# Optimization experiments

Hardware: AMD Instinct MI355X
Metric: run time of the kernel (lower is better)

## Reference

```python
import jax, jax.numpy as jnp
import numpy as np

B, N, V, F, H, O, NCONV = 4096, 64, 100, 128, 256, 1, 4
NEG_SLOPE = 0.01  # torch nn.LeakyReLU default


def leaky(x):
    return jnp.where(x >= 0, x, NEG_SLOPE * x)


def setup_inputs() -> dict:
    key = jax.random.key(0)
    ks = jax.random.split(key, 16)
    node_mat = jax.random.normal(ks[0], (B, N, V), dtype=jnp.float32)
    a = (jax.random.uniform(ks[1], (B, N, N)) < 0.15).astype(jnp.float32)
    adj_mat = jnp.maximum(a, jnp.swapaxes(a, 1, 2))
    s = 0.05
    params = dict(
        W_init=s * jax.random.normal(ks[2], (V, F), jnp.float32),
        b_init=jnp.zeros((F,), jnp.float32),
        W_conv=s * jax.random.normal(ks[3], (NCONV, F, F), jnp.float32),
        b_conv=jnp.zeros((NCONV, F), jnp.float32),
        W_fc0=s * jax.random.normal(ks[4], (F, H), jnp.float32),
        b_fc0=jnp.zeros((H,), jnp.float32),
        W_fc1=s * jax.random.normal(ks[5], (H, H), jnp.float32),
        b_fc1=jnp.zeros((H,), jnp.float32),
        W_out=s * jax.random.normal(ks[6], (H, O), jnp.float32),
        b_out=jnp.zeros((O,), jnp.float32),
    )
    return dict(node_mat=node_mat, adj_mat=adj_mat, **params)


def reference(node_mat, adj_mat, W_init, b_init, W_conv, b_conv,
              W_fc0, b_fc0, W_fc1, b_fc1, W_out, b_out):
    # init transform + LeakyReLU
    x = leaky(node_mat @ W_init + b_init)                      # [B, N, F]
    # degree-normalized adjacency: diag(1/deg) @ A == row-scale (exact same math
    # as the original eye-expand + double bmm, without the NxN diagonal matmul)
    deg = jnp.clip(adj_mat.sum(axis=-1, keepdims=True), 1.0, None)  # [B, N, 1]
    A_norm = adj_mat / deg                                     # [B, N, N]
    for i in range(W_conv.shape[0]):
        agg = jnp.einsum('bij,bjf->bif', A_norm, x)            # neighbor mean
        x = leaky(agg @ W_conv[i] + b_conv[i])
    # mean pooling over atoms
    g = x.mean(axis=1)                                         # [B, F]
    # fc head (dropout p=0 -> identity)
    h = leaky(g @ W_fc0 + b_fc0)
    h = leaky(h @ W_fc1 + b_fc1)
    return h @ W_out + b_out                                   # [B, O]
```

## Files before the change

kernel.cpp:

```cpp
#include <hip/hip_runtime.h>

#define NATOMS 64
#define VDIM 100
#define FDIM 128
#define HDIM 256
#define NCONV 4

typedef __bf16 bf16x8 __attribute__((ext_vector_type(8)));
typedef __bf16 bf16x4 __attribute__((ext_vector_type(4)));
typedef float f32x4 __attribute__((ext_vector_type(4)));

__device__ __forceinline__ float lrelu(float x) {
  return x >= 0.0f ? x : 0.01f * x;
}

__global__ void prep_weights(const float* __restrict__ Wi,
                             const float* __restrict__ Wc,
                             __bf16* __restrict__ WtI,
                             __bf16* __restrict__ WtC) {
  int idx = blockIdx.x * 256 + threadIdx.x;
  int e = idx & 7;
  int lane = (idx >> 3) & 63;
  int ks = (idx >> 9) & 3;
  int n16 = (idx >> 11) & 7;
  int l = idx >> 14;
  int n = n16 * 16 + (lane & 15);
  int k = ks * 32 + (lane >> 4) * 8 + e;
  if (l == 0) {
    WtI[idx] = (__bf16)(k < VDIM ? Wi[k * FDIM + n] : 0.0f);
  } else {
    WtC[(l - 1) * 16384 + (idx & 16383)] =
        (__bf16)Wc[(l - 1) * FDIM * FDIM + k * FDIM + n];
  }
}

template <bool PRODUCE_FRAG>
__device__ __forceinline__ void conv_step(
    const __bf16* __restrict__ Wt, const float* __restrict__ bias,
    const __bf16* __restrict__ sRow, bf16x8 xfrag[2][2], float psum[2],
    const int w, const int lane) {
  const int lr = lane & 15;
  const int g = lane >> 4;
  const int k0 = g * 8;
  f32x4 acc[2][4];
#pragma unroll
  for (int ni = 0; ni < 2; ++ni)
#pragma unroll
    for (int mi = 0; mi < 4; ++mi) acc[ni][mi] = {0.f, 0.f, 0.f, 0.f};
#pragma unroll
  for (int ks = 0; ks < 4; ++ks) {
    bf16x8 bfrag[2], afrag[4];
#pragma unroll
    for (int ni = 0; ni < 2; ++ni)
      bfrag[ni] = *(const bf16x8*)&Wt[(((2 * w + ni) * 4 + ks) * 64 + lane) * 8];
#pragma unroll
    for (int mi = 0; mi < 4; ++mi) {
      int m = mi * 16 + lr;
      afrag[mi] = *(const bf16x8*)&sRow[m * 128 + ((ks * 32 + k0) ^ ((m & 7) << 3))];
    }
#pragma unroll
    for (int ni = 0; ni < 2; ++ni)
#pragma unroll
      for (int mi = 0; mi < 4; ++mi)
        acc[ni][mi] = __builtin_amdgcn_mfma_f32_16x16x32_bf16(
            afrag[mi], bfrag[ni], acc[ni][mi], 0, 0, 0);
  }
#pragma unroll
  for (int ni = 0; ni < 2; ++ni) {
    float bv = bias[(2 * w + ni) * 16 + lr];
    if constexpr (PRODUCE_FRAG) {
      uint2 d[4];
#pragma unroll
      for (int mi = 0; mi < 4; ++mi) {
        bf16x4 o;
#pragma unroll
        for (int j = 0; j < 4; ++j) o[j] = (__bf16)lrelu(acc[ni][mi][j] + bv);
        d[mi] = __builtin_bit_cast(uint2, o);
      }
#pragma unroll
      for (int ksp = 0; ksp < 2; ++ksp) {
        unsigned r[4];
#pragma unroll
        for (int q = 0; q < 4; ++q) {
          int src = (2 * (g & 1) + (q >> 1)) * 16 + lr;
          unsigned lo = (q & 1) ? d[2 * ksp].y : d[2 * ksp].x;
          unsigned hi = (q & 1) ? d[2 * ksp + 1].y : d[2 * ksp + 1].x;
          unsigned va = (unsigned)__shfl((int)lo, src);
          unsigned vb = (unsigned)__shfl((int)hi, src);
          r[q] = (g >> 1) ? vb : va;
        }
        xfrag[ni][ksp] =
            __builtin_bit_cast(bf16x8, make_uint4(r[0], r[1], r[2], r[3]));
      }
    } else {
      float s = 0.f;
#pragma unroll
      for (int mi = 0; mi < 4; ++mi)
#pragma unroll
        for (int j = 0; j < 4; ++j) s += lrelu(acc[ni][mi][j] + bv);
      psum[ni] = s;
    }
  }
}

__device__ __forceinline__ void agg_step(const __bf16* __restrict__ sAdj,
                                         const bf16x8 xfrag[2][2],
                                         __bf16* __restrict__ sRow,
                                         const float rdgv[4], const int w,
                                         const int lane) {
  const int lr = lane & 15;
  const int g = lane >> 4;
  const int k0 = g * 8;
  f32x4 acc[2][4];
#pragma unroll
  for (int mi = 0; mi < 2; ++mi)
#pragma unroll
    for (int ni = 0; ni < 4; ++ni) acc[mi][ni] = {0.f, 0.f, 0.f, 0.f};
#pragma unroll
  for (int ks = 0; ks < 2; ++ks) {
    bf16x8 bfrag[4];
#pragma unroll
    for (int ni = 0; ni < 4; ++ni) {
      int n = ni * 16 + lr;
      bfrag[ni] = *(const bf16x8*)&sAdj[n * 64 + ((ks * 32 + k0) ^ ((n & 7) << 3))];
    }
#pragma unroll
    for (int mi = 0; mi < 2; ++mi)
#pragma unroll
      for (int ni = 0; ni < 4; ++ni)
        acc[mi][ni] = __builtin_amdgcn_mfma_f32_16x16x32_bf16(
            xfrag[mi][ks], bfrag[ni], acc[mi][ni], 0, 0, 0);
  }
#pragma unroll
  for (int ni = 0; ni < 4; ++ni) {
    float rv = rdgv[ni];
    int a = ni * 16 + lr;
#pragma unroll
    for (int mi = 0; mi < 2; ++mi) {
      int f0r = (2 * w + mi) * 16 + g * 4;
      bf16x4 o;
#pragma unroll
      for (int j = 0; j < 4; ++j) o[j] = (__bf16)(acc[mi][ni][j] * rv);
      *(bf16x4*)&sRow[a * 128 + (f0r ^ ((a & 7) << 3))] = o;
    }
  }
}

__launch_bounds__(256, 8)
__global__ void gcn_mfma(const float* __restrict__ node,
                         const float* __restrict__ adj,
                         const __bf16* __restrict__ WtI,
                         const __bf16* __restrict__ WtC,
                         const float* __restrict__ b_init,
                         const float* __restrict__ b_conv,
                         float* __restrict__ g_out) {
  __shared__ __align__(16) __bf16 sRow[NATOMS * FDIM];
  __shared__ __align__(16) __bf16 sAdj[NATOMS * NATOMS];
  __shared__ float sRdg[NATOMS];

  const int b = blockIdx.x;
  const int t = threadIdx.x;
  const int lane = t & 63;
  const int w = t >> 6;

  {
    const float* adjB = adj + (size_t)b * NATOMS * NATOMS;
#pragma unroll
    for (int half = 0; half < 2; ++half) {
      int n = (t >> 3) + half * 32;
      int gi = t & 7;
      float4 a0 = *(const float4*)&adjB[n * 64 + gi * 8];
      float4 a1 = *(const float4*)&adjB[n * 64 + gi * 8 + 4];
      bf16x8 v;
      v[0] = (__bf16)a0.x; v[1] = (__bf16)a0.y; v[2] = (__bf16)a0.z; v[3] = (__bf16)a0.w;
      v[4] = (__bf16)a1.x; v[5] = (__bf16)a1.y; v[6] = (__bf16)a1.z; v[7] = (__bf16)a1.w;
      *(bf16x8*)&sAdj[n * 64 + ((gi * 8) ^ ((n & 7) << 3))] = v;
      float p = a0.x + a0.y + a0.z + a0.w + a1.x + a1.y + a1.z + a1.w;
      p += __shfl_xor(p, 1); p += __shfl_xor(p, 2); p += __shfl_xor(p, 4);
      if (gi == 0) sRdg[n] = 1.0f / fmaxf(p, 1.0f);
    }
  }
  {
    const float* nodeB = node + (size_t)b * NATOMS * VDIM;
#pragma unroll
    for (int u0 = 0; u0 < 4; ++u0) {
      int u = t + 256 * u0;
      int n = u >> 4, gi = u & 15, kk = gi * 8;
      bf16x8 v;
      if (kk + 8 <= VDIM) {
        float4 a0 = *(const float4*)&nodeB[n * VDIM + kk];
        float4 a1 = *(const float4*)&nodeB[n * VDIM + kk + 4];
        v[0] = (__bf16)a0.x; v[1] = (__bf16)a0.y; v[2] = (__bf16)a0.z; v[3] = (__bf16)a0.w;
        v[4] = (__bf16)a1.x; v[5] = (__bf16)a1.y; v[6] = (__bf16)a1.z; v[7] = (__bf16)a1.w;
      } else {
#pragma unroll
        for (int i = 0; i < 8; ++i)
          v[i] = (__bf16)((kk + i < VDIM) ? nodeB[n * VDIM + kk + i] : 0.0f);
      }
      *(bf16x8*)&sRow[n * 128 + (kk ^ ((n & 7) << 3))] = v;
    }
  }
  __syncthreads();

  float rdgv[4];
#pragma unroll
  for (int ni = 0; ni < 4; ++ni) rdgv[ni] = sRdg[ni * 16 + (lane & 15)];

  bf16x8 xfrag[2][2];
  float psum[2];

  conv_step<true>(WtI, b_init, sRow, xfrag, psum, w, lane);
  __syncthreads();

#pragma unroll
  for (int l = 0; l < NCONV; ++l) {
    agg_step(sAdj, xfrag, sRow, rdgv, w, lane);
    __syncthreads();
    if (l < NCONV - 1) {
      conv_step<true>(WtC + l * 16384, b_conv + l * FDIM, sRow, xfrag, psum, w, lane);
      __syncthreads();
    } else {
      conv_step<false>(WtC + l * 16384, b_conv + l * FDIM, sRow, xfrag, psum, w, lane);
    }
  }

#pragma unroll
  for (int ni = 0; ni < 2; ++ni) {
    float s = psum[ni];
    s += __shfl_xor(s, 16);
    s += __shfl_xor(s, 32);
    if (lane < 16)
      g_out[(size_t)b * FDIM + (2 * w + ni) * 16 + lane] = s * (1.0f / 64.0f);
  }
}

__launch_bounds__(256, 2)
__global__ void head_fc(const float* __restrict__ g,
                        const float* __restrict__ W_fc0, const float* __restrict__ b_fc0,
                        const float* __restrict__ W_fc1, const float* __restrict__ b_fc1,
                        const float* __restrict__ W_out, const float* __restrict__ b_out,
                        float* __restrict__ out) {
  __shared__ __align__(16) float sG[16 * FDIM];
  __shared__ float sH[16 * (HDIM + 1)];
  __shared__ float sRed[4 * 16];

  const int t = threadIdx.x;
  const int lane = t & 63;
  const int w = t >> 6;
  const int r0 = blockIdx.x * 16;

  {
    const float4* gs = (const float4*)(g + (size_t)r0 * FDIM);
    float4* gd = (float4*)sG;
#pragma unroll
    for (int u = 0; u < 2; ++u) gd[t + 256 * u] = gs[t + 256 * u];
  }
  __syncthreads();

  float acc[16];
  {
    float bv = b_fc0[t];
#pragma unroll
    for (int r = 0; r < 16; ++r) acc[r] = bv;
    for (int k = 0; k < FDIM; ++k) {
      float wv = W_fc0[k * HDIM + t];
#pragma unroll
      for (int r = 0; r < 16; ++r) acc[r] += sG[r * FDIM + k] * wv;
    }
#pragma unroll
    for (int r = 0; r < 16; ++r) sH[r * (HDIM + 1) + t] = lrelu(acc[r]);
  }
  __syncthreads();

  {
    float bv = b_fc1[t];
#pragma unroll
    for (int r = 0; r < 16; ++r) acc[r] = bv;
    for (int k = 0; k < HDIM; ++k) {
      float wv = W_fc1[k * HDIM + t];
#pragma unroll
      for (int r = 0; r < 16; ++r) acc[r] += sH[r * (HDIM + 1) + k] * wv;
    }
    float wo = W_out[t];
#pragma unroll
    for (int r = 0; r < 16; ++r) acc[r] = lrelu(acc[r]) * wo;
  }
#pragma unroll
  for (int r = 0; r < 16; ++r) {
    float v = acc[r];
    v += __shfl_down(v, 32); v += __shfl_down(v, 16); v += __shfl_down(v, 8);
    v += __shfl_down(v, 4);  v += __shfl_down(v, 2);  v += __shfl_down(v, 1);
    if (lane == 0) sRed[w * 16 + r] = v;
  }
  __syncthreads();
  if (t < 16)
    out[r0 + t] = sRed[t] + sRed[16 + t] + sRed[32 + t] + sRed[48 + t] + b_out[0];
}

extern "C" void kernel_launch(void* const* d_in, const int* in_sizes, int n_in,
                              void* d_out, int out_size, void* d_ws, size_t ws_size,
                              hipStream_t stream) {
  (void)in_sizes; (void)n_in; (void)ws_size; (void)out_size;
  const float* node   = (const float*)d_in[0];
  const float* adj    = (const float*)d_in[1];
  const float* W_init = (const float*)d_in[2];
  const float* b_init = (const float*)d_in[3];
  const float* W_conv = (const float*)d_in[4];
  const float* b_conv = (const float*)d_in[5];
  const float* W_fc0  = (const float*)d_in[6];
  const float* b_fc0  = (const float*)d_in[7];
  const float* W_fc1  = (const float*)d_in[8];
  const float* b_fc1  = (const float*)d_in[9];
  const float* W_out  = (const float*)d_in[10];
  const float* b_out  = (const float*)d_in[11];
  float* out = (float*)d_out;

  __bf16* WtI = (__bf16*)d_ws;
  __bf16* WtC = WtI + 16384;
  float* g = (float*)((char*)d_ws + 160 * 1024);

  prep_weights<<<320, 256, 0, stream>>>(W_init, W_conv, WtI, WtC);
  gcn_mfma<<<4096, 256, 0, stream>>>(node, adj, WtI, WtC, b_init, b_conv, g);
  head_fc<<<256, 256, 0, stream>>>(g, W_fc0, b_fc0, W_fc1, b_fc1, W_out, b_out, out);
}
```

Before: 144.8 us.

## Use two waves per graph with 64-column tiles instead of four waves

New measurement: 158.0 us. 1.09x slower.

```diff
diff --git a/kernel.cpp b/kernel.cpp
--- a/kernel.cpp
+++ b/kernel.cpp
@@ -37,44 +37,44 @@
 template <bool PRODUCE_FRAG>
 __device__ __forceinline__ void conv_step(
     const __bf16* __restrict__ Wt, const float* __restrict__ bias,
-    const __bf16* __restrict__ sRow, bf16x8 xfrag[2][2], float psum[2],
-    const int w, const int lane) {
+    const __bf16* __restrict__ sRow, bf16x8 xfrag[4][2], float psum[4],
+    const int ww, const int lane) {
   const int lr = lane & 15;
   const int g = lane >> 4;
   const int k0 = g * 8;
-  f32x4 acc[2][4];
-#pragma unroll
-  for (int ni = 0; ni < 2; ++ni)
-#pragma unroll
-    for (int mi = 0; mi < 4; ++mi) acc[ni][mi] = {0.f, 0.f, 0.f, 0.f};
+  f32x4 acc[4][4];
+#pragma unroll
+  for (int mi = 0; mi < 4; ++mi)
+#pragma unroll
+    for (int ni = 0; ni < 4; ++ni) acc[mi][ni] = {0.f, 0.f, 0.f, 0.f};
 #pragma unroll
   for (int ks = 0; ks < 4; ++ks) {
-    bf16x8 bfrag[2], afrag[4];
-#pragma unroll
-    for (int ni = 0; ni < 2; ++ni)
-      bfrag[ni] = *(const bf16x8*)&Wt[(((2 * w + ni) * 4 + ks) * 64 + lane) * 8];
+    bf16x8 afrag[4], bfrag[4];
 #pragma unroll
     for (int mi = 0; mi < 4; ++mi) {
       int m = mi * 16 + lr;
       afrag[mi] = *(const bf16x8*)&sRow[m * 128 + ((ks * 32 + k0) ^ ((m & 7) << 3))];
     }
 #pragma unroll
-    for (int ni = 0; ni < 2; ++ni)
+    for (int ni = 0; ni < 4; ++ni)
+      bfrag[ni] = *(const bf16x8*)&Wt[(((ww * 4 + ni) * 4 + ks) * 64 + lane) * 8];
+#pragma unroll
+    for (int ni = 0; ni < 4; ++ni)
 #pragma unroll
       for (int mi = 0; mi < 4; ++mi)
-        acc[ni][mi] = __builtin_amdgcn_mfma_f32_16x16x32_bf16(
-            afrag[mi], bfrag[ni], acc[ni][mi], 0, 0, 0);
-  }
-#pragma unroll
-  for (int ni = 0; ni < 2; ++ni) {
-    float bv = bias[(2 * w + ni) * 16 + lr];
+        acc[mi][ni] = __builtin_amdgcn_mfma_f32_16x16x32_bf16(
+            afrag[mi], bfrag[ni], acc[mi][ni], 0, 0, 0);
+  }
+#pragma unroll
+  for (int ni = 0; ni < 4; ++ni) {
+    float bv = bias[(ww * 4 + ni) * 16 + lr];
     if constexpr (PRODUCE_FRAG) {
       uint2 d[4];
 #pragma unroll
       for (int mi = 0; mi < 4; ++mi) {
         bf16x4 o;
 #pragma unroll
-        for (int j = 0; j < 4; ++j) o[j] = (__bf16)lrelu(acc[ni][mi][j] + bv);
+        for (int j = 0; j < 4; ++j) o[j] = (__bf16)lrelu(acc[mi][ni][j] + bv);
         d[mi] = __builtin_bit_cast(uint2, o);
       }
 #pragma unroll
@@ -97,56 +97,56 @@
 #pragma unroll
       for (int mi = 0; mi < 4; ++mi)
 #pragma unroll
-        for (int j = 0; j < 4; ++j) s += lrelu(acc[ni][mi][j] + bv);
+        for (int j = 0; j < 4; ++j) s += lrelu(acc[mi][ni][j] + bv);
       psum[ni] = s;
     }
   }
 }
 
 __device__ __forceinline__ void agg_step(const __bf16* __restrict__ sAdj,
-                                         const bf16x8 xfrag[2][2],
+                                         const bf16x8 xfrag[4][2],
                                          __bf16* __restrict__ sRow,
-                                         const float rdgv[4], const int w,
+                                         const float rdgv[4], const int ww,
                                          const int lane) {
   const int lr = lane & 15;
   const int g = lane >> 4;
   const int k0 = g * 8;
-  f32x4 acc[2][4];
-#pragma unroll
-  for (int mi = 0; mi < 2; ++mi)
-#pragma unroll
-    for (int ni = 0; ni < 4; ++ni) acc[mi][ni] = {0.f, 0.f, 0.f, 0.f};
+  f32x4 acc[4][4];
+#pragma unroll
+  for (int fm = 0; fm < 4; ++fm)
+#pragma unroll
+    for (int an = 0; an < 4; ++an) acc[fm][an] = {0.f, 0.f, 0.f, 0.f};
 #pragma unroll
   for (int ks = 0; ks < 2; ++ks) {
     bf16x8 bfrag[4];
 #pragma unroll
-    for (int ni = 0; ni < 4; ++ni) {
-      int n = ni * 16 + lr;
-      bfrag[ni] = *(const bf16x8*)&sAdj[n * 64 + ((ks * 32 + k0) ^ ((n & 7) << 3))];
-    }
-#pragma unroll
-    for (int mi = 0; mi < 2; ++mi)
-#pragma unroll
-      for (int ni = 0; ni < 4; ++ni)
-        acc[mi][ni] = __builtin_amdgcn_mfma_f32_16x16x32_bf16(
-            xfrag[mi][ks], bfrag[ni], acc[mi][ni], 0, 0, 0);
-  }
-#pragma unroll
-  for (int ni = 0; ni < 4; ++ni) {
-    float rv = rdgv[ni];
-    int a = ni * 16 + lr;
-#pragma unroll
-    for (int mi = 0; mi < 2; ++mi) {
-      int f0r = (2 * w + mi) * 16 + g * 4;
+    for (int an = 0; an < 4; ++an) {
+      int n = an * 16 + lr;
+      bfrag[an] = *(const bf16x8*)&sAdj[n * 64 + ((ks * 32 + k0) ^ ((n & 7) << 3))];
+    }
+#pragma unroll
+    for (int fm = 0; fm < 4; ++fm)
+#pragma unroll
+      for (int an = 0; an < 4; ++an)
+        acc[fm][an] = __builtin_amdgcn_mfma_f32_16x16x32_bf16(
+            xfrag[fm][ks], bfrag[an], acc[fm][an], 0, 0, 0);
+  }
+#pragma unroll
+  for (int an = 0; an < 4; ++an) {
+    float rv = rdgv[an];
+    int a = an * 16 + lr;
+#pragma unroll
+    for (int fm = 0; fm < 4; ++fm) {
+      int f0r = (ww * 4 + fm) * 16 + g * 4;
       bf16x4 o;
 #pragma unroll
-      for (int j = 0; j < 4; ++j) o[j] = (__bf16)(acc[mi][ni][j] * rv);
+      for (int j = 0; j < 4; ++j) o[j] = (__bf16)(acc[fm][an][j] * rv);
       *(bf16x4*)&sRow[a * 128 + (f0r ^ ((a & 7) << 3))] = o;
     }
   }
 }
 
-__launch_bounds__(256, 8)
+__launch_bounds__(128, 2)
 __global__ void gcn_mfma(const float* __restrict__ node,
                          const float* __restrict__ adj,
                          const __bf16* __restrict__ WtI,
@@ -161,14 +161,15 @@
   const int b = blockIdx.x;
   const int t = threadIdx.x;
   const int lane = t & 63;
-  const int w = t >> 6;
+  const int ww = t >> 6;
+  const int lr = lane & 15;
 
   {
     const float* adjB = adj + (size_t)b * NATOMS * NATOMS;
 #pragma unroll
-    for (int half = 0; half < 2; ++half) {
-      int n = (t >> 3) + half * 32;
-      int gi = t & 7;
+    for (int u0 = 0; u0 < 4; ++u0) {
+      int u = t + 128 * u0;
+      int n = u >> 3, gi = u & 7;
       float4 a0 = *(const float4*)&adjB[n * 64 + gi * 8];
       float4 a1 = *(const float4*)&adjB[n * 64 + gi * 8 + 4];
       bf16x8 v;
@@ -183,8 +184,8 @@
   {
     const float* nodeB = node + (size_t)b * NATOMS * VDIM;
 #pragma unroll
-    for (int u0 = 0; u0 < 4; ++u0) {
-      int u = t + 256 * u0;
+    for (int u0 = 0; u0 < 8; ++u0) {
+      int u = t + 128 * u0;
       int n = u >> 4, gi = u & 15, kk = gi * 8;
       bf16x8 v;
       if (kk + 8 <= VDIM) {
@@ -204,33 +205,33 @@
 
   float rdgv[4];
 #pragma unroll
-  for (int ni = 0; ni < 4; ++ni) rdgv[ni] = sRdg[ni * 16 + (lane & 15)];
-
-  bf16x8 xfrag[2][2];
-  float psum[2];
-
-  conv_step<true>(WtI, b_init, sRow, xfrag, psum, w, lane);
+  for (int an = 0; an < 4; ++an) rdgv[an] = sRdg[an * 16 + lr];
+
+  bf16x8 xfrag[4][2];
+  float psum[4];
+
+  conv_step<true>(WtI, b_init, sRow, xfrag, psum, ww, lane);
   __syncthreads();
 
 #pragma unroll
   for (int l = 0; l < NCONV; ++l) {
-    agg_step(sAdj, xfrag, sRow, rdgv, w, lane);
+    agg_step(sAdj, xfrag, sRow, rdgv, ww, lane);
     __syncthreads();
     if (l < NCONV - 1) {
-      conv_step<true>(WtC + l * 16384, b_conv + l * FDIM, sRow, xfrag, psum, w, lane);
+      conv_step<true>(WtC + l * 16384, b_conv + l * FDIM, sRow, xfrag, psum, ww, lane);
       __syncthreads();
     } else {
-      conv_step<false>(WtC + l * 16384, b_conv + l * FDIM, sRow, xfrag, psum, w, lane);
-    }
-  }
-
-#pragma unroll
-  for (int ni = 0; ni < 2; ++ni) {
+      conv_step<false>(WtC + l * 16384, b_conv + l * FDIM, sRow, xfrag, psum, ww, lane);
+    }
+  }
+
+#pragma unroll
+  for (int ni = 0; ni < 4; ++ni) {
     float s = psum[ni];
     s += __shfl_xor(s, 16);
     s += __shfl_xor(s, 32);
     if (lane < 16)
-      g_out[(size_t)b * FDIM + (2 * w + ni) * 16 + lane] = s * (1.0f / 64.0f);
+      g_out[(size_t)b * FDIM + (ww * 4 + ni) * 16 + lane] = s * (1.0f / 64.0f);
   }
 }
 
@@ -320,6 +321,6 @@
   float* g = (float*)((char*)d_ws + 160 * 1024);
 
   prep_weights<<<320, 256, 0, stream>>>(W_init, W_conv, WtI, WtC);
-  gcn_mfma<<<4096, 256, 0, stream>>>(node, adj, WtI, WtC, b_init, b_conv, g);
+  gcn_mfma<<<4096, 128, 0, stream>>>(node, adj, WtI, WtC, b_init, b_conv, g);
   head_fc<<<256, 256, 0, stream>>>(g, W_fc0, b_fc0, W_fc1, b_fc1, W_out, b_out, out);
 }
```

## Process each graph with a single wavefront, keep adjacency in registers, drop barriers

Applied to the files above, without the earlier changes.

Measured after the change: 180.5 us. 24.7% more time.

```diff
diff --git a/kernel.cpp b/kernel.cpp
--- a/kernel.cpp
+++ b/kernel.cpp
@@ -35,118 +35,116 @@
 }
 
 template <bool PRODUCE_FRAG>
-__device__ __forceinline__ void conv_step(
+__device__ __forceinline__ void conv_one(
     const __bf16* __restrict__ Wt, const float* __restrict__ bias,
-    const __bf16* __restrict__ sRow, bf16x8 xfrag[2][2], float psum[2],
-    const int w, const int lane) {
+    const __bf16* __restrict__ sRow, bf16x8 xfrag[8][2], float psum[8],
+    const int lane) {
   const int lr = lane & 15;
   const int g = lane >> 4;
   const int k0 = g * 8;
-  f32x4 acc[2][4];
-#pragma unroll
-  for (int ni = 0; ni < 2; ++ni)
-#pragma unroll
-    for (int mi = 0; mi < 4; ++mi) acc[ni][mi] = {0.f, 0.f, 0.f, 0.f};
-#pragma unroll
-  for (int ks = 0; ks < 4; ++ks) {
-    bf16x8 bfrag[2], afrag[4];
+#pragma unroll
+  for (int nc = 0; nc < 4; ++nc) {
+    f32x4 acc[2][4];
 #pragma unroll
     for (int ni = 0; ni < 2; ++ni)
-      bfrag[ni] = *(const bf16x8*)&Wt[(((2 * w + ni) * 4 + ks) * 64 + lane) * 8];
-#pragma unroll
-    for (int mi = 0; mi < 4; ++mi) {
-      int m = mi * 16 + lr;
-      afrag[mi] = *(const bf16x8*)&sRow[m * 128 + ((ks * 32 + k0) ^ ((m & 7) << 3))];
-    }
-#pragma unroll
-    for (int ni = 0; ni < 2; ++ni)
-#pragma unroll
-      for (int mi = 0; mi < 4; ++mi)
-        acc[ni][mi] = __builtin_amdgcn_mfma_f32_16x16x32_bf16(
-            afrag[mi], bfrag[ni], acc[ni][mi], 0, 0, 0);
-  }
-#pragma unroll
-  for (int ni = 0; ni < 2; ++ni) {
-    float bv = bias[(2 * w + ni) * 16 + lr];
-    if constexpr (PRODUCE_FRAG) {
-      uint2 d[4];
+#pragma unroll
+      for (int mi = 0; mi < 4; ++mi) acc[ni][mi] = {0.f, 0.f, 0.f, 0.f};
+#pragma unroll
+    for (int ks = 0; ks < 4; ++ks) {
+      bf16x8 afrag[4], bfrag[2];
 #pragma unroll
       for (int mi = 0; mi < 4; ++mi) {
-        bf16x4 o;
-#pragma unroll
-        for (int j = 0; j < 4; ++j) o[j] = (__bf16)lrelu(acc[ni][mi][j] + bv);
-        d[mi] = __builtin_bit_cast(uint2, o);
-      }
-#pragma unroll
-      for (int ksp = 0; ksp < 2; ++ksp) {
-        unsigned r[4];
-#pragma unroll
-        for (int q = 0; q < 4; ++q) {
-          int src = (2 * (g & 1) + (q >> 1)) * 16 + lr;
-          unsigned lo = (q & 1) ? d[2 * ksp].y : d[2 * ksp].x;
-          unsigned hi = (q & 1) ? d[2 * ksp + 1].y : d[2 * ksp + 1].x;
-          unsigned va = (unsigned)__shfl((int)lo, src);
-          unsigned vb = (unsigned)__shfl((int)hi, src);
-          r[q] = (g >> 1) ? vb : va;
+        int m = mi * 16 + lr;
+        afrag[mi] = *(const bf16x8*)&sRow[m * 128 + ((ks * 32 + k0) ^ ((m & 7) << 3))];
+      }
+#pragma unroll
+      for (int ni = 0; ni < 2; ++ni)
+        bfrag[ni] = *(const bf16x8*)&Wt[(((nc * 2 + ni) * 4 + ks) * 64 + lane) * 8];
+#pragma unroll
+      for (int ni = 0; ni < 2; ++ni)
+#pragma unroll
+        for (int mi = 0; mi < 4; ++mi)
+          acc[ni][mi] = __builtin_amdgcn_mfma_f32_16x16x32_bf16(
+              afrag[mi], bfrag[ni], acc[ni][mi], 0, 0, 0);
+    }
+#pragma unroll
+    for (int ni = 0; ni < 2; ++ni) {
+      const int fm = nc * 2 + ni;
+      float bv = bias[fm * 16 + lr];
+      if constexpr (PRODUCE_FRAG) {
+        uint2 d[4];
+#pragma unroll
+        for (int mi = 0; mi < 4; ++mi) {
+          bf16x4 o;
+#pragma unroll
+          for (int j = 0; j < 4; ++j) o[j] = (__bf16)lrelu(acc[ni][mi][j] + bv);
+          d[mi] = __builtin_bit_cast(uint2, o);
         }
-        xfrag[ni][ksp] =
-            __builtin_bit_cast(bf16x8, make_uint4(r[0], r[1], r[2], r[3]));
-      }
-    } else {
-      float s = 0.f;
-#pragma unroll
-      for (int mi = 0; mi < 4; ++mi)
-#pragma unroll
-        for (int j = 0; j < 4; ++j) s += lrelu(acc[ni][mi][j] + bv);
-      psum[ni] = s;
-    }
-  }
-}
-
-__device__ __forceinline__ void agg_step(const __bf16* __restrict__ sAdj,
-                                         const bf16x8 xfrag[2][2],
-                                         __bf16* __restrict__ sRow,
-                                         const float rdgv[4], const int w,
-                                         const int lane) {
+#pragma unroll
+        for (int ksp = 0; ksp < 2; ++ksp) {
+          unsigned r[4];
+#pragma unroll
+          for (int q = 0; q < 4; ++q) {
+            int src = (2 * (g & 1) + (q >> 1)) * 16 + lr;
+            unsigned lo = (q & 1) ? d[2 * ksp].y : d[2 * ksp].x;
+            unsigned hi = (q & 1) ? d[2 * ksp + 1].y : d[2 * ksp + 1].x;
+            unsigned va = (unsigned)__shfl((int)lo, src);
+            unsigned vb = (unsigned)__shfl((int)hi, src);
+            r[q] = (g >> 1) ? vb : va;
+          }
+          xfrag[fm][ksp] =
+              __builtin_bit_cast(bf16x8, make_uint4(r[0], r[1], r[2], r[3]));
+        }
+      } else {
+        float s = 0.f;
+#pragma unroll
+        for (int mi = 0; mi < 4; ++mi)
+#pragma unroll
+          for (int j = 0; j < 4; ++j) s += lrelu(acc[ni][mi][j] + bv);
+        psum[fm] = s;
+      }
+    }
+  }
+}
+
+__device__ __forceinline__ void agg_one(const bf16x8 abfrag[4][2],
+                                        const bf16x8 xfrag[8][2],
+                                        __bf16* __restrict__ sRow,
+                                        const float rdgv[4], const int lane) {
   const int lr = lane & 15;
   const int g = lane >> 4;
-  const int k0 = g * 8;
-  f32x4 acc[2][4];
-#pragma unroll
-  for (int mi = 0; mi < 2; ++mi)
-#pragma unroll
-    for (int ni = 0; ni < 4; ++ni) acc[mi][ni] = {0.f, 0.f, 0.f, 0.f};
-#pragma unroll
-  for (int ks = 0; ks < 2; ++ks) {
-    bf16x8 bfrag[4];
-#pragma unroll
-    for (int ni = 0; ni < 4; ++ni) {
-      int n = ni * 16 + lr;
-      bfrag[ni] = *(const bf16x8*)&sAdj[n * 64 + ((ks * 32 + k0) ^ ((n & 7) << 3))];
-    }
-#pragma unroll
-    for (int mi = 0; mi < 2; ++mi)
-#pragma unroll
-      for (int ni = 0; ni < 4; ++ni)
-        acc[mi][ni] = __builtin_amdgcn_mfma_f32_16x16x32_bf16(
-            xfrag[mi][ks], bfrag[ni], acc[mi][ni], 0, 0, 0);
-  }
-#pragma unroll
-  for (int ni = 0; ni < 4; ++ni) {
-    float rv = rdgv[ni];
-    int a = ni * 16 + lr;
-#pragma unroll
-    for (int mi = 0; mi < 2; ++mi) {
-      int f0r = (2 * w + mi) * 16 + g * 4;
-      bf16x4 o;
-#pragma unroll
-      for (int j = 0; j < 4; ++j) o[j] = (__bf16)(acc[mi][ni][j] * rv);
-      *(bf16x4*)&sRow[a * 128 + (f0r ^ ((a & 7) << 3))] = o;
-    }
-  }
-}
-
-__launch_bounds__(256, 8)
+#pragma unroll
+  for (int fc = 0; fc < 4; ++fc) {
+    f32x4 acc[2][4];
+#pragma unroll
+    for (int fi = 0; fi < 2; ++fi)
+#pragma unroll
+      for (int an = 0; an < 4; ++an) acc[fi][an] = {0.f, 0.f, 0.f, 0.f};
+#pragma unroll
+    for (int ks = 0; ks < 2; ++ks)
+#pragma unroll
+      for (int fi = 0; fi < 2; ++fi)
+#pragma unroll
+        for (int an = 0; an < 4; ++an)
+          acc[fi][an] = __builtin_amdgcn_mfma_f32_16x16x32_bf16(
+              xfrag[fc * 2 + fi][ks], abfrag[an][ks], acc[fi][an], 0, 0, 0);
+#pragma unroll
+    for (int an = 0; an < 4; ++an) {
+      float rv = rdgv[an];
+      int a = an * 16 + lr;
+#pragma unroll
+      for (int fi = 0; fi < 2; ++fi) {
+        int f0r = (fc * 2 + fi) * 16 + g * 4;
+        bf16x4 o;
+#pragma unroll
+        for (int j = 0; j < 4; ++j) o[j] = (__bf16)(acc[fi][an][j] * rv);
+        *(bf16x4*)&sRow[a * 128 + (f0r ^ ((a & 7) << 3))] = o;
+      }
+    }
+  }
+}
+
+__launch_bounds__(64, 2)
 __global__ void gcn_mfma(const float* __restrict__ node,
                          const float* __restrict__ adj,
                          const __bf16* __restrict__ WtI,
@@ -155,36 +153,17 @@
                          const float* __restrict__ b_conv,
                          float* __restrict__ g_out) {
   __shared__ __align__(16) __bf16 sRow[NATOMS * FDIM];
-  __shared__ __align__(16) __bf16 sAdj[NATOMS * NATOMS];
-  __shared__ float sRdg[NATOMS];
 
   const int b = blockIdx.x;
-  const int t = threadIdx.x;
-  const int lane = t & 63;
-  const int w = t >> 6;
-
-  {
-    const float* adjB = adj + (size_t)b * NATOMS * NATOMS;
-#pragma unroll
-    for (int half = 0; half < 2; ++half) {
-      int n = (t >> 3) + half * 32;
-      int gi = t & 7;
-      float4 a0 = *(const float4*)&adjB[n * 64 + gi * 8];
-      float4 a1 = *(const float4*)&adjB[n * 64 + gi * 8 + 4];
-      bf16x8 v;
-      v[0] = (__bf16)a0.x; v[1] = (__bf16)a0.y; v[2] = (__bf16)a0.z; v[3] = (__bf16)a0.w;
-      v[4] = (__bf16)a1.x; v[5] = (__bf16)a1.y; v[6] = (__bf16)a1.z; v[7] = (__bf16)a1.w;
-      *(bf16x8*)&sAdj[n * 64 + ((gi * 8) ^ ((n & 7) << 3))] = v;
-      float p = a0.x + a0.y + a0.z + a0.w + a1.x + a1.y + a1.z + a1.w;
-      p += __shfl_xor(p, 1); p += __shfl_xor(p, 2); p += __shfl_xor(p, 4);
-      if (gi == 0) sRdg[n] = 1.0f / fmaxf(p, 1.0f);
-    }
-  }
+  const int lane = threadIdx.x;
+  const int lr = lane & 15;
+  const int g = lane >> 4;
+
   {
     const float* nodeB = node + (size_t)b * NATOMS * VDIM;
 #pragma unroll
-    for (int u0 = 0; u0 < 4; ++u0) {
-      int u = t + 256 * u0;
+    for (int u0 = 0; u0 < 16; ++u0) {
+      int u = lane + 64 * u0;
       int n = u >> 4, gi = u & 15, kk = gi * 8;
       bf16x8 v;
       if (kk + 8 <= VDIM) {
@@ -200,37 +179,51 @@
       *(bf16x8*)&sRow[n * 128 + (kk ^ ((n & 7) << 3))] = v;
     }
   }
-  __syncthreads();
-
+
+  bf16x8 abfrag[4][2];
   float rdgv[4];
-#pragma unroll
-  for (int ni = 0; ni < 4; ++ni) rdgv[ni] = sRdg[ni * 16 + (lane & 15)];
-
-  bf16x8 xfrag[2][2];
-  float psum[2];
-
-  conv_step<true>(WtI, b_init, sRow, xfrag, psum, w, lane);
-  __syncthreads();
-
+  {
+    const float* adjB = adj + (size_t)b * NATOMS * NATOMS;
+#pragma unroll
+    for (int an = 0; an < 4; ++an) {
+      int n = an * 16 + lr;
+      float deg = 0.f;
+#pragma unroll
+      for (int ks = 0; ks < 2; ++ks) {
+        float4 a0 = *(const float4*)&adjB[n * 64 + ks * 32 + g * 8];
+        float4 a1 = *(const float4*)&adjB[n * 64 + ks * 32 + g * 8 + 4];
+        bf16x8 v;
+        v[0] = (__bf16)a0.x; v[1] = (__bf16)a0.y; v[2] = (__bf16)a0.z; v[3] = (__bf16)a0.w;
+        v[4] = (__bf16)a1.x; v[5] = (__bf16)a1.y; v[6] = (__bf16)a1.z; v[7] = (__bf16)a1.w;
+        abfrag[an][ks] = v;
+        deg += a0.x + a0.y + a0.z + a0.w + a1.x + a1.y + a1.z + a1.w;
+      }
+      deg += __shfl_xor(deg, 16);
+      deg += __shfl_xor(deg, 32);
+      rdgv[an] = 1.0f / fmaxf(deg, 1.0f);
+    }
+  }
+
+  bf16x8 xfrag[8][2];
+  float psum[8];
+
+  conv_one<true>(WtI, b_init, sRow, xfrag, psum, lane);
 #pragma unroll
   for (int l = 0; l < NCONV; ++l) {
-    agg_step(sAdj, xfrag, sRow, rdgv, w, lane);
-    __syncthreads();
-    if (l < NCONV - 1) {
-      conv_step<true>(WtC + l * 16384, b_conv + l * FDIM, sRow, xfrag, psum, w, lane);
-      __syncthreads();
-    } else {
-      conv_step<false>(WtC + l * 16384, b_conv + l * FDIM, sRow, xfrag, psum, w, lane);
-    }
-  }
-
-#pragma unroll
-  for (int ni = 0; ni < 2; ++ni) {
-    float s = psum[ni];
+    agg_one(abfrag, xfrag, sRow, rdgv, lane);
+    if (l < NCONV - 1)
+      conv_one<true>(WtC + l * 16384, b_conv + l * FDIM, sRow, xfrag, psum, lane);
+    else
+      conv_one<false>(WtC + l * 16384, b_conv + l * FDIM, sRow, xfrag, psum, lane);
+  }
+
+#pragma unroll
+  for (int fm = 0; fm < 8; ++fm) {
+    float s = psum[fm];
     s += __shfl_xor(s, 16);
     s += __shfl_xor(s, 32);
     if (lane < 16)
-      g_out[(size_t)b * FDIM + (2 * w + ni) * 16 + lane] = s * (1.0f / 64.0f);
+      g_out[(size_t)b * FDIM + fm * 16 + lane] = s * (1.0f / 64.0f);
   }
 }
 
@@ -320,6 +313,6 @@
   float* g = (float*)((char*)d_ws + 160 * 1024);
 
   prep_weights<<<320, 256, 0, stream>>>(W_init, W_conv, WtI, WtC);
-  gcn_mfma<<<4096, 256, 0, stream>>>(node, adj, WtI, WtC, b_init, b_conv, g);
+  gcn_mfma<<<4096, 64, 0, stream>>>(node, adj, WtI, WtC, b_init, b_conv, g);
   head_fc<<<256, 256, 0, stream>>>(g, W_fc0, b_fc0, W_fc1, b_fc1, W_out, b_out, out);
 }
```

## Process four molecules per block with register prefetch of next molecule's inputs

Applied to the files above, without the earlier changes.

New measurement: 354.5 us. +144.8%, slower.

```diff
diff --git a/kernel.cpp b/kernel.cpp
--- a/kernel.cpp
+++ b/kernel.cpp
@@ -5,6 +5,7 @@
 #define FDIM 128
 #define HDIM 256
 #define NCONV 4
+#define MOLS_PER_BLOCK 4
 
 typedef __bf16 bf16x8 __attribute__((ext_vector_type(8)));
 typedef __bf16 bf16x4 __attribute__((ext_vector_type(4)));
@@ -146,7 +147,7 @@
   }
 }
 
-__launch_bounds__(256, 8)
+__launch_bounds__(256, 3)
 __global__ void gcn_mfma(const float* __restrict__ node,
                          const float* __restrict__ adj,
                          const __bf16* __restrict__ WtI,
@@ -158,19 +159,43 @@
   __shared__ __align__(16) __bf16 sAdj[NATOMS * NATOMS];
   __shared__ float sRdg[NATOMS];
 
-  const int b = blockIdx.x;
   const int t = threadIdx.x;
   const int lane = t & 63;
   const int w = t >> 6;
-
-  {
-    const float* adjB = adj + (size_t)b * NATOMS * NATOMS;
-#pragma unroll
-    for (int half = 0; half < 2; ++half) {
-      int n = (t >> 3) + half * 32;
-      int gi = t & 7;
-      float4 a0 = *(const float4*)&adjB[n * 64 + gi * 8];
-      float4 a1 = *(const float4*)&adjB[n * 64 + gi * 8 + 4];
+  const int lr = lane & 15;
+  const int b4 = blockIdx.x * MOLS_PER_BLOCK;
+
+  float4 nf[4][2];
+  float4 af[2][2];
+
+  auto issue_node = [&](int mol) {
+    const float* nodeB = node + (size_t)mol * NATOMS * VDIM;
+#pragma unroll
+    for (int s = 0; s < 4; ++s) {
+      int u = t + 256 * s;
+      int n = u >> 4, gi = u & 15, kk = gi * 8;
+      if (kk + 8 <= VDIM) {
+        nf[s][0] = *(const float4*)&nodeB[n * VDIM + kk];
+        nf[s][1] = *(const float4*)&nodeB[n * VDIM + kk + 4];
+      } else if (kk < VDIM) {
+        nf[s][0] = *(const float4*)&nodeB[n * VDIM + kk];
+      }
+    }
+  };
+  auto issue_adj = [&](int mol) {
+    const float* adjB = adj + (size_t)mol * NATOMS * NATOMS;
+#pragma unroll
+    for (int h = 0; h < 2; ++h) {
+      int n = (t >> 3) + h * 32, gi = t & 7;
+      af[h][0] = *(const float4*)&adjB[n * 64 + gi * 8];
+      af[h][1] = *(const float4*)&adjB[n * 64 + gi * 8 + 4];
+    }
+  };
+  auto convert_stage = [&]() {
+#pragma unroll
+    for (int h = 0; h < 2; ++h) {
+      int n = (t >> 3) + h * 32, gi = t & 7;
+      float4 a0 = af[h][0], a1 = af[h][1];
       bf16x8 v;
       v[0] = (__bf16)a0.x; v[1] = (__bf16)a0.y; v[2] = (__bf16)a0.z; v[3] = (__bf16)a0.w;
       v[4] = (__bf16)a1.x; v[5] = (__bf16)a1.y; v[6] = (__bf16)a1.z; v[7] = (__bf16)a1.w;
@@ -179,58 +204,70 @@
       p += __shfl_xor(p, 1); p += __shfl_xor(p, 2); p += __shfl_xor(p, 4);
       if (gi == 0) sRdg[n] = 1.0f / fmaxf(p, 1.0f);
     }
-  }
-  {
-    const float* nodeB = node + (size_t)b * NATOMS * VDIM;
-#pragma unroll
-    for (int u0 = 0; u0 < 4; ++u0) {
-      int u = t + 256 * u0;
+#pragma unroll
+    for (int s = 0; s < 4; ++s) {
+      int u = t + 256 * s;
       int n = u >> 4, gi = u & 15, kk = gi * 8;
       bf16x8 v;
       if (kk + 8 <= VDIM) {
-        float4 a0 = *(const float4*)&nodeB[n * VDIM + kk];
-        float4 a1 = *(const float4*)&nodeB[n * VDIM + kk + 4];
+        float4 a0 = nf[s][0], a1 = nf[s][1];
         v[0] = (__bf16)a0.x; v[1] = (__bf16)a0.y; v[2] = (__bf16)a0.z; v[3] = (__bf16)a0.w;
         v[4] = (__bf16)a1.x; v[5] = (__bf16)a1.y; v[6] = (__bf16)a1.z; v[7] = (__bf16)a1.w;
+      } else if (kk < VDIM) {
+        float4 a0 = nf[s][0];
+        v[0] = (__bf16)a0.x; v[1] = (__bf16)a0.y; v[2] = (__bf16)a0.z; v[3] = (__bf16)a0.w;
+        v[4] = (__bf16)0.f; v[5] = (__bf16)0.f; v[6] = (__bf16)0.f; v[7] = (__bf16)0.f;
       } else {
 #pragma unroll
-        for (int i = 0; i < 8; ++i)
-          v[i] = (__bf16)((kk + i < VDIM) ? nodeB[n * VDIM + kk + i] : 0.0f);
+        for (int i = 0; i < 8; ++i) v[i] = (__bf16)0.f;
       }
       *(bf16x8*)&sRow[n * 128 + (kk ^ ((n & 7) << 3))] = v;
     }
-  }
-  __syncthreads();
-
-  float rdgv[4];
-#pragma unroll
-  for (int ni = 0; ni < 4; ++ni) rdgv[ni] = sRdg[ni * 16 + (lane & 15)];
-
-  bf16x8 xfrag[2][2];
-  float psum[2];
-
-  conv_step<true>(WtI, b_init, sRow, xfrag, psum, w, lane);
-  __syncthreads();
-
-#pragma unroll
-  for (int l = 0; l < NCONV; ++l) {
-    agg_step(sAdj, xfrag, sRow, rdgv, w, lane);
+  };
+
+  issue_node(b4);
+  issue_adj(b4);
+
+  for (int it = 0; it < MOLS_PER_BLOCK; ++it) {
+    convert_stage();
     __syncthreads();
-    if (l < NCONV - 1) {
-      conv_step<true>(WtC + l * 16384, b_conv + l * FDIM, sRow, xfrag, psum, w, lane);
+
+    float rdgv[4];
+#pragma unroll
+    for (int ni = 0; ni < 4; ++ni) rdgv[ni] = sRdg[ni * 16 + lr];
+
+    if (it < MOLS_PER_BLOCK - 1) {
+      issue_node(b4 + it + 1);
+      issue_adj(b4 + it + 1);
+    }
+
+    bf16x8 xfrag[2][2];
+    float psum[2];
+
+    conv_step<true>(WtI, b_init, sRow, xfrag, psum, w, lane);
+    __syncthreads();
+
+#pragma unroll
+    for (int l = 0; l < NCONV; ++l) {
+      agg_step(sAdj, xfrag, sRow, rdgv, w, lane);
       __syncthreads();
-    } else {
-      conv_step<false>(WtC + l * 16384, b_conv + l * FDIM, sRow, xfrag, psum, w, lane);
-    }
-  }
-
-#pragma unroll
-  for (int ni = 0; ni < 2; ++ni) {
-    float s = psum[ni];
-    s += __shfl_xor(s, 16);
-    s += __shfl_xor(s, 32);
-    if (lane < 16)
-      g_out[(size_t)b * FDIM + (2 * w + ni) * 16 + lane] = s * (1.0f / 64.0f);
+      if (l < NCONV - 1) {
+        conv_step<true>(WtC + l * 16384, b_conv + l * FDIM, sRow, xfrag, psum, w, lane);
+        __syncthreads();
+      } else {
+        conv_step<false>(WtC + l * 16384, b_conv + l * FDIM, sRow, xfrag, psum, w, lane);
+      }
+    }
+
+#pragma unroll
+    for (int ni = 0; ni < 2; ++ni) {
+      float s = psum[ni];
+      s += __shfl_xor(s, 16);
+      s += __shfl_xor(s, 32);
+      if (lane < 16)
+        g_out[(size_t)(b4 + it) * FDIM + (2 * w + ni) * 16 + lane] = s * (1.0f / 64.0f);
+    }
+    __syncthreads();
   }
 }
 
@@ -320,6 +357,7 @@
   float* g = (float*)((char*)d_ws + 160 * 1024);
 
   prep_weights<<<320, 256, 0, stream>>>(W_init, W_conv, WtI, WtC);
-  gcn_mfma<<<4096, 256, 0, stream>>>(node, adj, WtI, WtC, b_init, b_conv, g);
+  gcn_mfma<<<4096 / MOLS_PER_BLOCK, 256, 0, stream>>>(node, adj, WtI, WtC,
+                                                      b_init, b_conv, g);
   head_fc<<<256, 256, 0, stream>>>(g, W_fc0, b_fc0, W_fc1, b_fc1, W_out, b_out, out);
 }
```
